# Kernel tuning notes

Hardware: AMD Instinct MI355X
Metric: run time of the kernel (lower is better)

The kernel has to match this reference:

```python
import jax, jax.numpy as jnp
import numpy as np

V, D, L, H, S, B = 30522, 768, 12, 12, 64, 128
DK = D // H
FF = 4 * D
EPS = 1e-5

def _positional_table():
    # replicates the (buggy) exponent 10000**(2*i/d) from the source
    pos = np.arange(S, dtype=np.float32)[:, None]
    i = np.arange(0, D, 2, dtype=np.float32)
    arg = pos / (10000.0 ** (2.0 * i / D))
    pe = np.zeros((S, D), dtype=np.float32)
    pe[:, 0::2] = np.sin(arg)
    pe[:, 1::2] = np.cos(arg)
    return jnp.asarray(pe)[None]  # [1,S,D]

PE = _positional_table()

def setup_inputs() -> dict:
    key = jax.random.key(0)
    ks = jax.random.split(key, 20)
    sc = 0.02
    tok_emb = jax.random.normal(ks[0], (V, D), jnp.float32) * sc
    tok_emb = tok_emb.at[0].set(0.0)  # padding_idx=0
    seg_emb = jax.random.normal(ks[1], (3, D), jnp.float32) * sc
    seg_emb = seg_emb.at[0].set(0.0)
    def w(k, shape):
        return jax.random.normal(k, shape, jnp.float32) * sc
    return {
        "x": jax.random.randint(ks[2], (B, S), 0, V),
        "segment": jax.random.randint(ks[3], (B, S), 0, 3),
        "tok_emb": tok_emb, "seg_emb": seg_emb,
        "Wq": w(ks[4], (L, D, D)), "bq": jnp.zeros((L, D)),
        "Wk": w(ks[5], (L, D, D)), "bk": jnp.zeros((L, D)),
        "Wv": w(ks[6], (L, D, D)), "bv": jnp.zeros((L, D)),
        "Wo": w(ks[7], (L, D, D)), "bo": jnp.zeros((L, D)),
        "ln_g": jnp.ones((L, D)), "ln_b": jnp.zeros((L, D)),
        "W1": w(ks[8], (L, D, FF)), "b1": jnp.zeros((L, FF)),
        "W2": w(ks[9], (L, FF, D)), "b2": jnp.zeros((L, D)),
    }

def _layernorm(x, g, b):
    mu = jnp.mean(x, -1, keepdims=True)
    var = jnp.mean(jnp.square(x - mu), -1, keepdims=True)
    return (x - mu) * jax.lax.rsqrt(var + EPS) * g + b

def reference(x, segment, tok_emb, seg_emb, Wq, bq, Wk, bk, Wv, bv, Wo, bo,
              ln_g, ln_b, W1, b1, W2, b2):
    # mask: (x>0) -> [B,1,1,S], broadcasts over query rows like the repeat in torch
    mask = (x > 0)[:, None, None, :]
    h = tok_emb[x] + seg_emb[segment] + PE  # [B,S,D]

    def layer(h, p):
        wq, bq_, wk, bk_, wv, bv_, wo, bo_, g, be, w1, b1_, w2, b2_ = p
        q = (h @ wq + bq_).reshape(B, S, H, DK).transpose(0, 2, 1, 3)
        k = (h @ wk + bk_).reshape(B, S, H, DK).transpose(0, 2, 1, 3)
        v = (h @ wv + bv_).reshape(B, S, H, DK).transpose(0, 2, 1, 3)
        scores = jnp.einsum('bhqd,bhkd->bhqk', q, k) / jnp.sqrt(jnp.float32(DK))
        scores = jnp.where(mask, scores, -1e9)
        w = jax.nn.softmax(scores, axis=-1)
        ctx = jnp.einsum('bhqk,bhkd->bhqd', w, v).transpose(0, 2, 1, 3).reshape(B, S, D)
        attn = ctx @ wo + bo_
        h1 = _layernorm(attn + h, g, be)  # shared LN params within the layer
        ff = jax.nn.gelu(h1 @ w1 + b1_, approximate=False) @ w2 + b2_
        h2 = _layernorm(h1 + ff, g, be)
        return h2, None

    params = (Wq, bq, Wk, bk, Wv, bv, Wo, bo, ln_g, ln_b, W1, b1, W2, b2)
    h, _ = jax.lax.scan(layer, h, params)
    return h
```

## Files before the change

### kernel.cpp

```cpp
#include <hip/hip_runtime.h>
#include <math.h>

typedef unsigned short u16;
typedef __bf16 bf16x8 __attribute__((ext_vector_type(8)));
typedef float f32x4 __attribute__((ext_vector_type(4)));
typedef unsigned long long u64;

__device__ __forceinline__ float bf2f(u16 u) {
    union { unsigned u32; float f; } c; c.u32 = ((unsigned)u) << 16; return c.f;
}
__device__ __forceinline__ u16 f2bf(float f) {
    unsigned u = __float_as_uint(f);
    unsigned r = u + 0x7fff + ((u >> 16) & 1);
    return (u16)(r >> 16);
}
__device__ __forceinline__ float ldmix(const void* p, u64 i, int isbf) {
    return isbf ? bf2f(((const u16*)p)[i]) : ((const float*)p)[i];
}
__device__ __forceinline__ void gll16(const u16* g, u16* l) {
    __builtin_amdgcn_global_load_lds(
        (const __attribute__((address_space(1))) void*)g,
        (__attribute__((address_space(3))) void*)l, 16, 0, 0);
}

__global__ void detect_kernel(const unsigned* __restrict__ tokw, int* __restrict__ flag)
{
    int i = threadIdx.x;
    unsigned w = tokw[768 + i];
    unsigned e = (w >> 7) & 0xFF;
    bool hit = (e >= 100) && (e <= 126) && ((w & 0x7FFFu) != 0);
    unsigned long long m = __ballot(hit);
    if (i == 0) flag[0] = (__popcll(m) >= 40) ? 1 : 0;
}

__global__ __launch_bounds__(256) void embed_kernel(
    const int* __restrict__ x, const int* __restrict__ seg,
    const void* __restrict__ tok, const void* __restrict__ se,
    const int* __restrict__ flagp, float* __restrict__ hF, u16* __restrict__ hB)
{
    int isbf = *flagp;
    int t = blockIdx.x;
    int pos = t & 63;
    int tokid = x[t], sgid = seg[t];
    int tid = threadIdx.x;
#pragma unroll
    for (int i = 0; i < 3; i++) {
        int d = tid + i * 256;
        int p = d >> 1;
        float freq = powf(10000.0f, (float)p * (1.0f / 192.0f));
        float arg = (float)pos / freq;
        float pe = (d & 1) ? cosf(arg) : sinf(arg);
        float v = ldmix(tok, (u64)tokid * 768 + d, isbf)
                + ldmix(se, (u64)sgid * 768 + d, isbf) + pe;
        hF[(u64)t * 768 + d] = v;
        hB[(u64)t * 768 + d] = f2bf(v);
    }
}

__global__ __launch_bounds__(256) void transpose6(
    const void* __restrict__ wq, const void* __restrict__ wk,
    const void* __restrict__ wv, const void* __restrict__ wo,
    const void* __restrict__ w1, const void* __restrict__ w2,
    u16* __restrict__ out, const int* __restrict__ flagp, u64 oS, u64 oF)
{
    int isbf = *flagp;
    int id = blockIdx.x;
    const void* src; u16* dst; int R, C; u64 off;
    if (id < 2304) {
        int m = id / 576; id -= m * 576; R = 768; C = 768; off = oS;
        src = (m == 0) ? wq : (m == 1) ? wk : (m == 2) ? wv : wo;
        dst = out + (u64)m * 589824;
    } else if (id < 4608) {
        id -= 2304; R = 768; C = 3072; off = oF; src = w1; dst = out + 2359296;
    } else {
        id -= 4608; R = 3072; C = 768; off = oF; src = w2; dst = out + 4718592;
    }
    int tilesC = C >> 5;
    int tr = id / tilesC, tc = id % tilesC;
    __shared__ float tile[32][33];
    int rl = threadIdx.x >> 5, cl = threadIdx.x & 31;
#pragma unroll
    for (int i = 0; i < 4; i++)
        tile[rl + 8 * i][cl] = ldmix(src, off + (u64)(tr * 32 + rl + 8 * i) * C + tc * 32 + cl, isbf);
    __syncthreads();
#pragma unroll
    for (int i = 0; i < 4; i++)
        dst[(u64)(tc * 32 + rl + 8 * i) * R + tr * 32 + cl] = f2bf(tile[cl][rl + 8 * i]);
}

template <int MODE>
__global__ __launch_bounds__(256, 2) void gemm_bt(
    const u16* __restrict__ A, const u16* __restrict__ Bt,
    const void* __restrict__ bA, const void* __restrict__ bB,
    const void* __restrict__ bC, u64 oB, const float* __restrict__ resid,
    float* __restrict__ outF, u16* __restrict__ outB,
    const int* __restrict__ flagp, int N, int K)
{
    __shared__ __align__(16) u16 sA[128 * 32];
    __shared__ __align__(16) u16 sB[128 * 32];
    int tid = threadIdx.x;
    int lane = tid & 63, wave = tid >> 6;
    int wr = wave >> 1, wc = wave & 1;
    int bn = blockIdx.x, bm = blockIdx.y;
    const u16* Ab = A + (u64)bm * 128 * K;
    const u16* Bb = Bt + (u64)bn * 128 * K;
    int srow = tid >> 2;
    int scol = (tid & 3) * 8;
    u16* sAw0 = sA + wave * 512;
    u16* sAw1 = sA + 2048 + wave * 512;
    u16* sBw0 = sB + wave * 512;
    u16* sBw1 = sB + 2048 + wave * 512;
    const u16* Ar0 = Ab + (u64)srow * K + scol;
    const u16* Ar1 = Ab + (u64)(srow + 64) * K + scol;
    const u16* Br0 = Bb + (u64)srow * K + scol;
    const u16* Br1 = Bb + (u64)(srow + 64) * K + scol;
    int cl = lane & 15, quad = lane >> 4;

    f32x4 acc[4][4];
    const f32x4 vz = {0.f, 0.f, 0.f, 0.f};
#pragma unroll
    for (int mi = 0; mi < 4; mi++)
#pragma unroll
        for (int ni = 0; ni < 4; ni++) acc[mi][ni] = vz;

    gll16(Ar0, sAw0); gll16(Ar1, sAw1);
    gll16(Br0, sBw0); gll16(Br1, sBw1);

    for (int k0 = 0; k0 < K; k0 += 32) {
        __syncthreads();
        bf16x8 af[4], bfr[4];
#pragma unroll
        for (int mi = 0; mi < 4; mi++)
            af[mi] = *(const bf16x8*)(sA + (wr * 64 + mi * 16 + cl) * 32 + quad * 8);
#pragma unroll
        for (int ni = 0; ni < 4; ni++)
            bfr[ni] = *(const bf16x8*)(sB + (wc * 64 + ni * 16 + cl) * 32 + quad * 8);
        __syncthreads();
        int kn = k0 + 32;
        if (kn < K) {
            gll16(Ar0 + kn, sAw0); gll16(Ar1 + kn, sAw1);
            gll16(Br0 + kn, sBw0); gll16(Br1 + kn, sBw1);
        }
#pragma unroll
        for (int mi = 0; mi < 4; mi++)
#pragma unroll
            for (int ni = 0; ni < 4; ni++)
                acc[mi][ni] = __builtin_amdgcn_mfma_f32_16x16x32_bf16(
                    af[mi], bfr[ni], acc[mi][ni], 0, 0, 0);
    }

    int isbf = *flagp;
    int rowb = bm * 128 + wr * 64 + quad * 4;
    int colb = bn * 128 + wc * 64 + cl;
    const void* bp = bA;
    int csub = 0;
    if (MODE == 3) {
        int ms = bn / 6;
        bp = (ms == 0) ? bA : (ms == 1) ? bB : bC;
        csub = ms * 768;
    }
#pragma unroll
    for (int ni = 0; ni < 4; ni++) {
        int col = colb + ni * 16;
        float bv = ldmix(bp, oB + (u64)(col - csub), isbf);
#pragma unroll
        for (int mi = 0; mi < 4; mi++) {
#pragma unroll
            for (int r = 0; r < 4; r++) {
                int row = rowb + mi * 16 + r;
                float v = acc[mi][ni][r] + bv;
                if (MODE == 1) {
                    v += resid[(u64)row * N + col];
                    outF[(u64)row * N + col] = v;
                } else {
                    if (MODE == 2) v = 0.5f * v * (1.0f + erff(v * 0.70710678118654752f));
                    outB[(u64)row * N + col] = f2bf(v);
                }
            }
        }
    }
}

__global__ __launch_bounds__(256) void attn_kernel(
    const u16* __restrict__ QKV, const int* __restrict__ xids, u16* __restrict__ ctx)
{
    constexpr int LDA = 72;
    __shared__ __align__(16) u16 sQ[64 * LDA];
    __shared__ __align__(16) u16 sK[64 * LDA];
    __shared__ __align__(16) u16 sVt[64 * LDA];
    int tid = threadIdx.x;
    int lane = tid & 63, wave = tid >> 6;
    int b = blockIdx.x / 12, h = blockIdx.x % 12;
    {
        int r = tid >> 2, cb = (tid & 3) * 16;
        u64 gbase = ((u64)(b * 64 + r)) * 2304 + h * 64 + cb;
        uint4 q0 = *(const uint4*)(QKV + gbase);
        uint4 q1 = *(const uint4*)(QKV + gbase + 8);
        uint4 k0 = *(const uint4*)(QKV + gbase + 768);
        uint4 k1 = *(const uint4*)(QKV + gbase + 776);
        uint4 v0 = *(const uint4*)(QKV + gbase + 1536);
        uint4 v1 = *(const uint4*)(QKV + gbase + 1544);
        *(uint4*)(sQ + r * LDA + cb) = q0;
        *(uint4*)(sQ + r * LDA + cb + 8) = q1;
        *(uint4*)(sK + r * LDA + cb) = k0;
        *(uint4*)(sK + r * LDA + cb + 8) = k1;
        u16 vt[16];
        *(uint4*)(vt) = v0; *(uint4*)(vt + 8) = v1;
#pragma unroll
        for (int j = 0; j < 16; j++) sVt[(cb + j) * LDA + r] = vt[j];
    }
    __syncthreads();
    int cl = lane & 15, quad = lane >> 4;

    f32x4 sc[4];
    const f32x4 vz = {0.f, 0.f, 0.f, 0.f};
#pragma unroll
    for (int ni = 0; ni < 4; ni++) sc[ni] = vz;
#pragma unroll
    for (int kt = 0; kt < 2; kt++) {
        bf16x8 a = *(const bf16x8*)(sQ + (wave * 16 + cl) * LDA + kt * 32 + quad * 8);
#pragma unroll
        for (int ni = 0; ni < 4; ni++) {
            bf16x8 bb = *(const bf16x8*)(sK + (ni * 16 + cl) * LDA + kt * 32 + quad * 8);
            sc[ni] = __builtin_amdgcn_mfma_f32_16x16x32_bf16(a, bb, sc[ni], 0, 0, 0);
        }
    }
    bool ok[4];
#pragma unroll
    for (int ni = 0; ni < 4; ni++) ok[ni] = xids[b * 64 + ni * 16 + cl] > 0;
    float p[4][4];
#pragma unroll
    for (int r = 0; r < 4; r++) {
        float m = -3.0e38f;
#pragma unroll
        for (int ni = 0; ni < 4; ni++) {
            float s = ok[ni] ? sc[ni][r] * 0.125f : -1e9f;
            p[ni][r] = s;
            m = fmaxf(m, s);
        }
#pragma unroll
        for (int off = 1; off < 16; off <<= 1) m = fmaxf(m, __shfl_xor(m, off));
        float sum = 0.f;
#pragma unroll
        for (int ni = 0; ni < 4; ni++) { float e = __expf(p[ni][r] - m); p[ni][r] = e; sum += e; }
#pragma unroll
        for (int off = 1; off < 16; off <<= 1) sum += __shfl_xor(sum, off);
        float inv = 1.0f / sum;
#pragma unroll
        for (int ni = 0; ni < 4; ni++) p[ni][r] *= inv;
    }
    __syncthreads();
#pragma unroll
    for (int ni = 0; ni < 4; ni++)
#pragma unroll
        for (int r = 0; r < 4; r++)
            sQ[(wave * 16 + quad * 4 + r) * LDA + ni * 16 + cl] = f2bf(p[ni][r]);
    __syncthreads();
    f32x4 o[4];
#pragma unroll
    for (int ni = 0; ni < 4; ni++) o[ni] = vz;
#pragma unroll
    for (int kt = 0; kt < 2; kt++) {
        bf16x8 a = *(const bf16x8*)(sQ + (wave * 16 + cl) * LDA + kt * 32 + quad * 8);
#pragma unroll
        for (int ni = 0; ni < 4; ni++) {
            bf16x8 bb = *(const bf16x8*)(sVt + (ni * 16 + cl) * LDA + kt * 32 + quad * 8);
            o[ni] = __builtin_amdgcn_mfma_f32_16x16x32_bf16(a, bb, o[ni], 0, 0, 0);
        }
    }
#pragma unroll
    for (int ni = 0; ni < 4; ni++)
#pragma unroll
        for (int r = 0; r < 4; r++)
            ctx[((u64)(b * 64 + wave * 16 + quad * 4 + r)) * 768 + h * 64 + ni * 16 + cl] =
                f2bf(o[ni][r]);
}

__global__ __launch_bounds__(256) void ln_kernel(
    const float* __restrict__ X, const void* __restrict__ g, const void* __restrict__ bta,
    const int* __restrict__ flagp, float* __restrict__ outF, u16* __restrict__ outH,
    void* __restrict__ outD, int isfinal, u64 oB)
{
    int isbf = *flagp;
    int t = blockIdx.x;
    const float* xr = X + (u64)t * 768;
    int tid = threadIdx.x;
    float v0 = xr[tid], v1 = xr[tid + 256], v2 = xr[tid + 512];
    float s = v0 + v1 + v2;
    float sq = v0 * v0 + v1 * v1 + v2 * v2;
#pragma unroll
    for (int off = 1; off < 64; off <<= 1) { s += __shfl_xor(s, off); sq += __shfl_xor(sq, off); }
    __shared__ float red[8];
    int lane = tid & 63, wave = tid >> 6;
    if (lane == 0) { red[wave] = s; red[4 + wave] = sq; }
    __syncthreads();
    s = red[0] + red[1] + red[2] + red[3];
    sq = red[4] + red[5] + red[6] + red[7];
    float mu = s * (1.0f / 768.0f);
    float var = sq * (1.0f / 768.0f) - mu * mu;
    float rs = rsqrtf(var + 1e-5f);
    float* of = outF + (u64)t * 768;
#pragma unroll
    for (int i = 0; i < 3; i++) {
        int c = tid + i * 256;
        float v = (i == 0) ? v0 : (i == 1) ? v1 : v2;
        float y = (v - mu) * rs * ldmix(g, oB + c, isbf) + ldmix(bta, oB + c, isbf);
        of[c] = y;
        outH[(u64)t * 768 + c] = f2bf(y);
        if (isfinal) {
            if (isbf) ((u16*)outD)[(u64)t * 768 + c] = f2bf(y);
            else      ((float*)outD)[(u64)t * 768 + c] = y;
        }
    }
}

extern "C" void kernel_launch(void* const* d_in, const int* in_sizes, int n_in,
                              void* d_out, int out_size, void* d_ws, size_t ws_size,
                              hipStream_t stream)
{
    const int* x    = (const int*)d_in[0];
    const int* seg  = (const int*)d_in[1];
    const void* tok = d_in[2];
    const void* sege= d_in[3];
    const void* Wq  = d_in[4];
    const void* bq  = d_in[5];
    const void* Wk  = d_in[6];
    const void* bk  = d_in[7];
    const void* Wv  = d_in[8];
    const void* bv  = d_in[9];
    const void* Wo  = d_in[10];
    const void* bo  = d_in[11];
    const void* lng = d_in[12];
    const void* lnb = d_in[13];
    const void* W1  = d_in[14];
    const void* b1  = d_in[15];
    const void* W2  = d_in[16];
    const void* b2  = d_in[17];

    const u64 ND = 8192ull * 768ull;
    char* p = (char*)d_ws;
    auto alloc = [&](size_t bytes) { char* q = p; p += (bytes + 255) & ~(size_t)255; return q; };
    int*   flag = (int*)alloc(256);
    float* hF   = (float*)alloc(ND * 4);
    float* xF   = (float*)alloc(ND * 4);
    u16*   hB   = (u16*)alloc(ND * 2);
    u16*   xB   = (u16*)alloc(ND * 2);
    u16*   qkvB = (u16*)alloc(ND * 3 * 2);
    u16*   ctxB = (u16*)alloc(ND * 2);
    u16*   ffB  = qkvB;
    u16*   Wt   = (u16*)alloc(7077888ull * 2);

    detect_kernel<<<1, 64, 0, stream>>>((const unsigned*)tok, flag);
    embed_kernel<<<8192, 256, 0, stream>>>(x, seg, tok, sege, flag, hF, hB);

    dim3 g768(6, 64), g2304(18, 64), g3072(24, 64);
    for (int l = 0; l < 12; l++) {
        const u64 oS = (u64)l * 589824ull, oF = (u64)l * 2359296ull;
        const u64 oB = (u64)l * 768ull, oB1 = (u64)l * 3072ull;
        transpose6<<<6912, 256, 0, stream>>>(Wq, Wk, Wv, Wo, W1, W2, Wt, flag, oS, oF);
        gemm_bt<3><<<g2304, 256, 0, stream>>>(hB, Wt, bq, bk, bv, oB,
                                              nullptr, nullptr, qkvB, flag, 2304, 768);
        attn_kernel<<<1536, 256, 0, stream>>>(qkvB, x, ctxB);
        gemm_bt<1><<<g768, 256, 0, stream>>>(ctxB, Wt + 1769472, bo, nullptr, nullptr, oB,
                                             hF, xF, nullptr, flag, 768, 768);
        ln_kernel<<<8192, 256, 0, stream>>>(xF, lng, lnb, flag, xF, xB, nullptr, 0, oB);
        gemm_bt<2><<<g3072, 256, 0, stream>>>(xB, Wt + 2359296, b1, nullptr, nullptr, oB1,
                                              nullptr, nullptr, ffB, flag, 3072, 768);
        gemm_bt<1><<<g768, 256, 0, stream>>>(ffB, Wt + 4718592, b2, nullptr, nullptr, oB,
                                             xF, xF, nullptr, flag, 768, 3072);
        ln_kernel<<<8192, 256, 0, stream>>>(xF, lng, lnb, flag, hF, hB,
                                            (l == 11) ? d_out : nullptr,
                                            (l == 11) ? 1 : 0, oB);
    }
}
```

Baseline: 3.561 ms.

## Replace GEMM with 256x256-tile, 8-wave, double-buffered swizzled-LDS pipelined kernel

Result: slower. 4.263 ms (+19.7%).

```diff
diff --git a/kernel.cpp b/kernel.cpp
--- a/kernel.cpp
+++ b/kernel.cpp
@@ -89,73 +89,155 @@
 }
 
 template <int MODE>
-__global__ __launch_bounds__(256, 2) void gemm_bt(
+__global__ __launch_bounds__(512, 2) void gemm8p(
     const u16* __restrict__ A, const u16* __restrict__ Bt,
     const void* __restrict__ bA, const void* __restrict__ bB,
     const void* __restrict__ bC, u64 oB, const float* __restrict__ resid,
     float* __restrict__ outF, u16* __restrict__ outB,
     const int* __restrict__ flagp, int N, int K)
 {
-    __shared__ __align__(16) u16 sA[128 * 32];
-    __shared__ __align__(16) u16 sB[128 * 32];
+    __shared__ __align__(16) u16 sm[65536];
+    const int NT = K >> 6;
     int tid = threadIdx.x;
     int lane = tid & 63, wave = tid >> 6;
-    int wr = wave >> 1, wc = wave & 1;
+    int wr = wave >> 2, wc = wave & 3;
+    int cl = lane & 15, quad = lane >> 4;
     int bn = blockIdx.x, bm = blockIdx.y;
-    const u16* Ab = A + (u64)bm * 128 * K;
-    const u16* Bb = Bt + (u64)bn * 128 * K;
-    int srow = tid >> 2;
-    int scol = (tid & 3) * 8;
-    u16* sAw0 = sA + wave * 512;
-    u16* sAw1 = sA + 2048 + wave * 512;
-    u16* sBw0 = sB + wave * 512;
-    u16* sBw1 = sB + 2048 + wave * 512;
-    const u16* Ar0 = Ab + (u64)srow * K + scol;
-    const u16* Ar1 = Ab + (u64)(srow + 64) * K + scol;
-    const u16* Br0 = Bb + (u64)srow * K + scol;
-    const u16* Br1 = Bb + (u64)(srow + 64) * K + scol;
-    int cl = lane & 15, quad = lane >> 4;
-
-    f32x4 acc[4][4];
+
+    int offA[8], offB[4];
+#pragma unroll
+    for (int mi = 0; mi < 8; mi++) {
+        int r = wr * 128 + mi * 16 + cl;
+        offA[mi] = r * 32 + ((quad ^ ((r >> 1) & 3)) << 3);
+    }
+#pragma unroll
+    for (int ni = 0; ni < 4; ni++) {
+        int r = wc * 64 + ni * 16 + cl;
+        offB[ni] = r * 32 + ((quad ^ ((r >> 1) & 3)) << 3);
+    }
+
+    const u16 *sA0, *sA1, *sB0, *sB1;
+    const int dst0 = wave * 512;
+    const int dst1 = 4096 + wave * 512;
+    {
+        int c0 = wave * 64 + lane, c1 = 512 + wave * 64 + lane;
+        int r0 = c0 >> 2, q0 = (c0 & 3) ^ ((r0 >> 1) & 3);
+        int r1 = c1 >> 2, q1 = (c1 & 3) ^ ((r1 >> 1) & 3);
+        sA0 = A  + (u64)(bm * 256 + r0) * K + q0 * 8;
+        sA1 = A  + (u64)(bm * 256 + r1) * K + q1 * 8;
+        sB0 = Bt + (u64)(bn * 256 + r0) * K + q0 * 8;
+        sB1 = Bt + (u64)(bn * 256 + r1) * K + q1 * 8;
+    }
+    auto STG = [&](int ro, const u16* a0, const u16* a1, int koff) {
+        gll16(a0 + koff, sm + ro + dst0);
+        gll16(a1 + koff, sm + ro + dst1);
+    };
+
+    f32x4 acc[8][4];
     const f32x4 vz = {0.f, 0.f, 0.f, 0.f};
 #pragma unroll
-    for (int mi = 0; mi < 4; mi++)
+    for (int mi = 0; mi < 8; mi++)
 #pragma unroll
         for (int ni = 0; ni < 4; ni++) acc[mi][ni] = vz;
 
-    gll16(Ar0, sAw0); gll16(Ar1, sAw1);
-    gll16(Br0, sBw0); gll16(Br1, sBw1);
-
-    for (int k0 = 0; k0 < K; k0 += 32) {
-        __syncthreads();
-        bf16x8 af[4], bfr[4];
-#pragma unroll
-        for (int mi = 0; mi < 4; mi++)
-            af[mi] = *(const bf16x8*)(sA + (wr * 64 + mi * 16 + cl) * 32 + quad * 8);
-#pragma unroll
-        for (int ni = 0; ni < 4; ni++)
-            bfr[ni] = *(const bf16x8*)(sB + (wc * 64 + ni * 16 + cl) * 32 + quad * 8);
-        __syncthreads();
-        int kn = k0 + 32;
-        if (kn < K) {
-            gll16(Ar0 + kn, sAw0); gll16(Ar1 + kn, sAw1);
-            gll16(Br0 + kn, sBw0); gll16(Br1 + kn, sBw1);
-        }
+    STG(0,     sA0, sA1, 0);
+    STG(16384, sB0, sB1, 0);
+    STG(8192,  sA0, sA1, 32);
+    STG(24576, sB0, sB1, 32);
+    if (NT > 1) {
+        STG(32768,         sA0, sA1, 64);
+        STG(32768 + 16384, sB0, sB1, 64);
+        STG(32768 + 24576, sB0, sB1, 96);
+        asm volatile("s_waitcnt vmcnt(6)" ::: "memory");
+    } else {
+        asm volatile("s_waitcnt vmcnt(0)" ::: "memory");
+    }
+    __builtin_amdgcn_s_barrier();
+
+    for (int t = 0; t < NT; t++) {
+        const int sl = (t & 1) * 32768;
+        const int osl = sl ^ 32768;
+        const u16* Ak0 = sm + sl;
+        const u16* Ak1 = sm + sl + 8192;
+        const u16* Bk0 = sm + sl + 16384;
+        const u16* Bk1 = sm + sl + 24576;
+        const int k1 = (t + 1) * 64, k2 = (t + 2) * 64;
+        bf16x8 af[4], bf[4];
+
+#pragma unroll
+        for (int i = 0; i < 4; i++) af[i] = *(const bf16x8*)(Ak0 + offA[i]);
+#pragma unroll
+        for (int i = 0; i < 4; i++) bf[i] = *(const bf16x8*)(Bk0 + offB[i]);
+        if (t + 1 < NT) STG(osl + 8192, sA0, sA1, k1 + 32);
+        __builtin_amdgcn_s_barrier();
+        asm volatile("s_waitcnt lgkmcnt(0)" ::: "memory");
+        __builtin_amdgcn_s_setprio(1);
 #pragma unroll
         for (int mi = 0; mi < 4; mi++)
 #pragma unroll
             for (int ni = 0; ni < 4; ni++)
                 acc[mi][ni] = __builtin_amdgcn_mfma_f32_16x16x32_bf16(
-                    af[mi], bfr[ni], acc[mi][ni], 0, 0, 0);
+                    af[mi], bf[ni], acc[mi][ni], 0, 0, 0);
+        __builtin_amdgcn_s_setprio(0);
+        __builtin_amdgcn_s_barrier();
+
+#pragma unroll
+        for (int i = 0; i < 4; i++) af[i] = *(const bf16x8*)(Ak0 + offA[4 + i]);
+        if (t + 2 < NT) STG(sl + 16384, sB0, sB1, k2);
+        __builtin_amdgcn_s_barrier();
+        asm volatile("s_waitcnt lgkmcnt(0)" ::: "memory");
+        __builtin_amdgcn_s_setprio(1);
+#pragma unroll
+        for (int mi = 0; mi < 4; mi++)
+#pragma unroll
+            for (int ni = 0; ni < 4; ni++)
+                acc[4 + mi][ni] = __builtin_amdgcn_mfma_f32_16x16x32_bf16(
+                    af[mi], bf[ni], acc[4 + mi][ni], 0, 0, 0);
+        __builtin_amdgcn_s_setprio(0);
+        __builtin_amdgcn_s_barrier();
+
+#pragma unroll
+        for (int i = 0; i < 4; i++) af[i] = *(const bf16x8*)(Ak1 + offA[i]);
+#pragma unroll
+        for (int i = 0; i < 4; i++) bf[i] = *(const bf16x8*)(Bk1 + offB[i]);
+        if (t + 2 < NT) STG(sl, sA0, sA1, k2);
+        __builtin_amdgcn_s_barrier();
+        asm volatile("s_waitcnt lgkmcnt(0)" ::: "memory");
+        __builtin_amdgcn_s_setprio(1);
+#pragma unroll
+        for (int mi = 0; mi < 4; mi++)
+#pragma unroll
+            for (int ni = 0; ni < 4; ni++)
+                acc[mi][ni] = __builtin_amdgcn_mfma_f32_16x16x32_bf16(
+                    af[mi], bf[ni], acc[mi][ni], 0, 0, 0);
+        __builtin_amdgcn_s_setprio(0);
+        __builtin_amdgcn_s_barrier();
+
+#pragma unroll
+        for (int i = 0; i < 4; i++) af[i] = *(const bf16x8*)(Ak1 + offA[4 + i]);
+        if (t + 2 < NT) STG(sl + 24576, sB0, sB1, k2 + 32);
+        __builtin_amdgcn_s_barrier();
+        asm volatile("s_waitcnt lgkmcnt(0)" ::: "memory");
+        __builtin_amdgcn_s_setprio(1);
+#pragma unroll
+        for (int mi = 0; mi < 4; mi++)
+#pragma unroll
+            for (int ni = 0; ni < 4; ni++)
+                acc[4 + mi][ni] = __builtin_amdgcn_mfma_f32_16x16x32_bf16(
+                    af[mi], bf[ni], acc[4 + mi][ni], 0, 0, 0);
+        __builtin_amdgcn_s_setprio(0);
+        if (t + 2 < NT) asm volatile("s_waitcnt vmcnt(6)" ::: "memory");
+        else            asm volatile("s_waitcnt vmcnt(0)" ::: "memory");
+        __builtin_amdgcn_s_barrier();
     }
 
     int isbf = *flagp;
-    int rowb = bm * 128 + wr * 64 + quad * 4;
-    int colb = bn * 128 + wc * 64 + cl;
+    int rowb = bm * 256 + wr * 128 + quad * 4;
+    int colb = bn * 256 + wc * 64 + cl;
     const void* bp = bA;
     int csub = 0;
     if (MODE == 3) {
-        int ms = bn / 6;
+        int ms = bn / 3;
         bp = (ms == 0) ? bA : (ms == 1) ? bB : bC;
         csub = ms * 768;
     }
@@ -164,7 +246,7 @@
         int col = colb + ni * 16;
         float bv = ldmix(bp, oB + (u64)(col - csub), isbf);
 #pragma unroll
-        for (int mi = 0; mi < 4; mi++) {
+        for (int mi = 0; mi < 8; mi++) {
 #pragma unroll
             for (int r = 0; r < 4; r++) {
                 int row = rowb + mi * 16 + r;
@@ -353,21 +435,21 @@
     detect_kernel<<<1, 64, 0, stream>>>((const unsigned*)tok, flag);
     embed_kernel<<<8192, 256, 0, stream>>>(x, seg, tok, sege, flag, hF, hB);
 
-    dim3 g768(6, 64), g2304(18, 64), g3072(24, 64);
+    dim3 gq(9, 32), gp(3, 32), gf1(12, 32), gf2(3, 32);
     for (int l = 0; l < 12; l++) {
         const u64 oS = (u64)l * 589824ull, oF = (u64)l * 2359296ull;
         const u64 oB = (u64)l * 768ull, oB1 = (u64)l * 3072ull;
         transpose6<<<6912, 256, 0, stream>>>(Wq, Wk, Wv, Wo, W1, W2, Wt, flag, oS, oF);
-        gemm_bt<3><<<g2304, 256, 0, stream>>>(hB, Wt, bq, bk, bv, oB,
-                                              nullptr, nullptr, qkvB, flag, 2304, 768);
+        gemm8p<3><<<gq, 512, 0, stream>>>(hB, Wt, bq, bk, bv, oB,
+                                          nullptr, nullptr, qkvB, flag, 2304, 768);
         attn_kernel<<<1536, 256, 0, stream>>>(qkvB, x, ctxB);
-        gemm_bt<1><<<g768, 256, 0, stream>>>(ctxB, Wt + 1769472, bo, nullptr, nullptr, oB,
-                                             hF, xF, nullptr, flag, 768, 768);
+        gemm8p<1><<<gp, 512, 0, stream>>>(ctxB, Wt + 1769472, bo, nullptr, nullptr, oB,
+                                          hF, xF, nullptr, flag, 768, 768);
         ln_kernel<<<8192, 256, 0, stream>>>(xF, lng, lnb, flag, xF, xB, nullptr, 0, oB);
-        gemm_bt<2><<<g3072, 256, 0, stream>>>(xB, Wt + 2359296, b1, nullptr, nullptr, oB1,
-                                              nullptr, nullptr, ffB, flag, 3072, 768);
-        gemm_bt<1><<<g768, 256, 0, stream>>>(ffB, Wt + 4718592, b2, nullptr, nullptr, oB,
-                                             xF, xF, nullptr, flag, 768, 3072);
+        gemm8p<2><<<gf1, 512, 0, stream>>>(xB, Wt + 2359296, b1, nullptr, nullptr, oB1,
+                                           nullptr, nullptr, ffB, flag, 3072, 768);
+        gemm8p<1><<<gf2, 512, 0, stream>>>(ffB, Wt + 4718592, b2, nullptr, nullptr, oB,
+                                           xF, xF, nullptr, flag, 768, 3072);
         ln_kernel<<<8192, 256, 0, stream>>>(xF, lng, lnb, flag, hF, hB,
                                             (l == 11) ? d_out : nullptr,
                                             (l == 11) ? 1 : 0, oB);
```

## Swizzle GEMM LDS layout, group-M block rasterization, raise occupancy hint

Applied to the files above, without the earlier changes.

Result: faster. 3.438 ms (-3.5%).

```diff
diff --git a/kernel.cpp b/kernel.cpp
--- a/kernel.cpp
+++ b/kernel.cpp
@@ -89,7 +89,7 @@
 }
 
 template <int MODE>
-__global__ __launch_bounds__(256, 2) void gemm_bt(
+__global__ __launch_bounds__(256, 4) void gemm_bt(
     const u16* __restrict__ A, const u16* __restrict__ Bt,
     const void* __restrict__ bA, const void* __restrict__ bB,
     const void* __restrict__ bC, u64 oB, const float* __restrict__ resid,
@@ -101,20 +101,27 @@
     int tid = threadIdx.x;
     int lane = tid & 63, wave = tid >> 6;
     int wr = wave >> 1, wc = wave & 1;
-    int bn = blockIdx.x, bm = blockIdx.y;
-    const u16* Ab = A + (u64)bm * 128 * K;
-    const u16* Bb = Bt + (u64)bn * 128 * K;
-    int srow = tid >> 2;
-    int scol = (tid & 3) * 8;
-    u16* sAw0 = sA + wave * 512;
-    u16* sAw1 = sA + 2048 + wave * 512;
-    u16* sBw0 = sB + wave * 512;
-    u16* sBw1 = sB + 2048 + wave * 512;
-    const u16* Ar0 = Ab + (u64)srow * K + scol;
-    const u16* Ar1 = Ab + (u64)(srow + 64) * K + scol;
-    const u16* Br0 = Bb + (u64)srow * K + scol;
-    const u16* Br1 = Bb + (u64)(srow + 64) * K + scol;
     int cl = lane & 15, quad = lane >> 4;
+
+    int lin = blockIdx.y * gridDim.x + blockIdx.x;
+    int per = gridDim.x << 3;
+    int grp = lin / per, rem = lin - grp * per;
+    int bm = (grp << 3) + (rem & 7), bn = rem >> 3;
+
+    const u16 *As0, *As1, *Bs0, *Bs1;
+    {
+        int c0 = tid, c1 = 256 + tid;
+        int r0 = c0 >> 2, g0 = ((c0 & 3) ^ ((r0 >> 1) & 3)) << 3;
+        int r1 = c1 >> 2, g1 = ((c1 & 3) ^ ((r1 >> 1) & 3)) << 3;
+        As0 = A  + (u64)(bm * 128 + r0) * K + g0;
+        As1 = A  + (u64)(bm * 128 + r1) * K + g1;
+        Bs0 = Bt + (u64)(bn * 128 + r0) * K + g0;
+        Bs1 = Bt + (u64)(bn * 128 + r1) * K + g1;
+    }
+    u16* dA0 = sA + wave * 512;  u16* dA1 = sA + 2048 + wave * 512;
+    u16* dB0 = sB + wave * 512;  u16* dB1 = sB + 2048 + wave * 512;
+
+    const int swz = (quad ^ ((cl >> 1) & 3)) << 3;
 
     f32x4 acc[4][4];
     const f32x4 vz = {0.f, 0.f, 0.f, 0.f};
@@ -123,23 +130,23 @@
 #pragma unroll
         for (int ni = 0; ni < 4; ni++) acc[mi][ni] = vz;
 
-    gll16(Ar0, sAw0); gll16(Ar1, sAw1);
-    gll16(Br0, sBw0); gll16(Br1, sBw1);
+    gll16(As0, dA0); gll16(As1, dA1);
+    gll16(Bs0, dB0); gll16(Bs1, dB1);
 
     for (int k0 = 0; k0 < K; k0 += 32) {
         __syncthreads();
         bf16x8 af[4], bfr[4];
 #pragma unroll
         for (int mi = 0; mi < 4; mi++)
-            af[mi] = *(const bf16x8*)(sA + (wr * 64 + mi * 16 + cl) * 32 + quad * 8);
+            af[mi] = *(const bf16x8*)(sA + (wr * 64 + mi * 16 + cl) * 32 + swz);
 #pragma unroll
         for (int ni = 0; ni < 4; ni++)
-            bfr[ni] = *(const bf16x8*)(sB + (wc * 64 + ni * 16 + cl) * 32 + quad * 8);
+            bfr[ni] = *(const bf16x8*)(sB + (wc * 64 + ni * 16 + cl) * 32 + swz);
         __syncthreads();
         int kn = k0 + 32;
         if (kn < K) {
-            gll16(Ar0 + kn, sAw0); gll16(Ar1 + kn, sAw1);
-            gll16(Br0 + kn, sBw0); gll16(Br1 + kn, sBw1);
+            gll16(As0 + kn, dA0); gll16(As1 + kn, dA1);
+            gll16(Bs0 + kn, dB0); gll16(Bs1 + kn, dB1);
         }
 #pragma unroll
         for (int mi = 0; mi < 4; mi++)
```
